# Kernel tuning notes

Hardware: AMD Instinct MI355X
Metric: run time of the kernel (lower is better)

## Reference

```python
import jax, jax.numpy as jnp
import numpy as np

MERGE_K = 3   # merge_kernel
DS_K = 3      # ds_kernel (avg-pool kernel)
STRIDE = 2


def _unfold(x, kernel, stride):
    """Torch-style F.pad + unfold(2).unfold(3): x [N,C,H,W] -> [N,Ho,Wo,K,C],
    K = kernel**2 in row-major (dh, dw) order, padding = kernel//2 with zeros."""
    pad = kernel // 2
    N, C, H, W = x.shape
    Ho, Wo = H // stride, W // stride
    xp = jnp.pad(x, ((0, 0), (0, 0), (pad, pad), (pad, pad)))
    pats = [
        xp[:, :, di:di + stride * (Ho - 1) + 1:stride,
               dj:dj + stride * (Wo - 1) + 1:stride]
        for di in range(kernel) for dj in range(kernel)
    ]
    p = jnp.stack(pats, axis=-1)          # [N,C,Ho,Wo,K]
    return p.transpose(0, 2, 3, 4, 1)     # [N,Ho,Wo,K,C]


def setup_inputs() -> dict:
    key = jax.random.key(0)
    x = jax.random.normal(key, (32, 768, 56, 56), dtype=jnp.float32)
    return {"x": x}


def reference(x):
    # compute_kq=False: k = q = x
    # AvgPool2d(3, stride=2, padding=1), count_include_pad=True -> mean over
    # zero-padded 3x3 windows == mean over K axis of the unfold.
    q = _unfold(x, DS_K, STRIDE).mean(axis=3)   # [N,Ho,Wo,C]
    kv = _unfold(x, MERGE_K, STRIDE)            # [N,Ho,Wo,K,C]; k and v are identical unfolds of x
    scores = jnp.einsum('nhwc,nhwkc->nhwk', q, kv) / MERGE_K  # divide by merge_kernel (=3), per source
    attn = jax.nn.softmax(scores, axis=-1)      # [N,Ho,Wo,K]
    y = jnp.einsum('nhwk,nhwkc->nhwc', attn, kv)  # weighted merge
    return y.transpose(0, 3, 1, 2)              # [N,C,Ho,Wo]
```

## Files before the change

### kernel.cpp

```cpp
#include <hip/hip_runtime.h>


constexpr int N_  = 32;
constexpr int C_  = 768;
constexpr int H_  = 56;
constexpr int W_  = 56;
constexpr int HO_ = 28;
constexpr int WO_ = 28;
constexpr int HW_ = H_ * W_;

constexpr int SC      = 16;
constexpr int NSUB    = C_ / SC;
constexpr int TILE_F4 = 768;

#define WAITV3() do { asm volatile("s_waitcnt vmcnt(3)" ::: "memory"); \
                      __builtin_amdgcn_sched_barrier(0); } while (0)
#define WAITV0() do { asm volatile("s_waitcnt vmcnt(0)" ::: "memory"); \
                      __builtin_amdgcn_sched_barrier(0); } while (0)
#define RAWBAR() do { asm volatile("" ::: "memory"); __builtin_amdgcn_s_barrier(); \
                      __builtin_amdgcn_sched_barrier(0); } while (0)

__global__ __launch_bounds__(256)
void fused_kernel(const float* __restrict__ x, float* __restrict__ out) {
    __shared__ float4 bufs[3][TILE_F4];
    __shared__ float  sred[8 * 252];
    __shared__ float  attn_s[252];

    const int tid  = threadIdx.x;
    const int blk  = blockIdx.x;
    const int n    = blk / HO_;
    const int ho   = blk - n * HO_;
    const int row0 = 2 * ho - 1;
    const int lane = tid & 63;
    const int wv   = tid >> 6;

    int goff[3], lds4[3];
#pragma unroll
    for (int j = 0; j < 3; ++j) {
        int q  = wv + 4 * j;
        int i  = q * 64 + lane;
        int ii = i > 671 ? 671 : i;
        int c  = ii / 42;
        int rem = ii - c * 42;
        int r  = rem / 14;
        int kk = rem - r * 14;
        int grow = row0 + r; if (grow < 0) grow = 0;
        goff[j] = c * HW_ + grow * W_ + 4 * kk;
        lds4[j] = q * 64;
    }

    const float* xb = x + (size_t)n * C_ * HW_;
    auto stage = [&](int sub, int bsel) {
        const float* xs = xb + (size_t)sub * (SC * HW_);
        float4* tb = &bufs[bsel][0];
#pragma unroll
        for (int j = 0; j < 3; ++j)
            __builtin_amdgcn_global_load_lds(
                (const __attribute__((address_space(1))) unsigned int*)(xs + goff[j]),
                (__attribute__((address_space(3))) unsigned int*)(tb + lds4[j]),
                16, 0, 0);
    };

    const int g   = tid >> 5;
    const int wo  = tid & 31;
    const bool act = wo < WO_;
    const float mt  = (ho > 0) ? 1.f : 0.f;
    const float ml  = (wo > 0) ? 1.f : 0.f;
    const float mtl = mt * ml;

    float acc[9];
#pragma unroll
    for (int k = 0; k < 9; ++k) acc[k] = 0.f;

    stage(0, 0);
    stage(1, 1);
    WAITV3();
    RAWBAR();

    for (int t = 0; t < 48; ++t) {
        int s = t + 2;
        stage(s < 48 ? s : s - 48, s % 3);
        const float* cur = (const float*)&bufs[t % 3][0];
        if (act) {
#pragma unroll
            for (int cc = 0; cc < 2; ++cc) {
                const float* tp = cur + (g * 2 + cc) * 168 + 2 * wo - 1;
                float w0 = tp[0]   * mtl, w1 = tp[1]   * mt, w2 = tp[2]   * mt;
                float w3 = tp[56]  * ml,  w4 = tp[57],      w5 = tp[58];
                float w6 = tp[112] * ml,  w7 = tp[113],     w8 = tp[114];
                float q = ((w0 + w1) + (w2 + w3)) + ((w4 + w5) + (w6 + w7)) + w8;
                acc[0] += q * w0; acc[1] += q * w1; acc[2] += q * w2;
                acc[3] += q * w3; acc[4] += q * w4; acc[5] += q * w5;
                acc[6] += q * w6; acc[7] += q * w7; acc[8] += q * w8;
            }
        }
        WAITV3();
        RAWBAR();
    }

    if (act) {
#pragma unroll
        for (int k = 0; k < 9; ++k) sred[g * 252 + wo * 9 + k] = acc[k];
    }
    __syncthreads();
    if (tid < 252) {
        float t = 0.f;
#pragma unroll
        for (int g2 = 0; g2 < 8; ++g2) t += sred[g2 * 252 + tid];
        attn_s[tid] = t * (1.f / 27.f);
    }
    __syncthreads();
    if (tid < WO_) {
        float* s = &attn_s[tid * 9];
        float v[9];
#pragma unroll
        for (int k = 0; k < 9; ++k) v[k] = s[k];
        float m = v[0];
#pragma unroll
        for (int k = 1; k < 9; ++k) m = fmaxf(m, v[k]);
        float d = 0.f;
#pragma unroll
        for (int k = 0; k < 9; ++k) { v[k] = __expf(v[k] - m); d += v[k]; }
        float inv = 1.f / d;
#pragma unroll
        for (int k = 0; k < 9; ++k) s[k] = v[k] * inv;
    }
    __syncthreads();

    const int cA = tid / 28, wA = tid - cA * 28;
    const int iB = tid + 256;
    const int cB = iB / 28, wB = iB - cB * 28;
    const bool actB = iB < 448;
    const float mlA = (wA > 0) ? 1.f : 0.f;
    const float mlB = (wB > 0) ? 1.f : 0.f;
    float* ob = out + (size_t)n * C_ * (HO_ * WO_) + (size_t)ho * WO_;

    for (int t = 48; t < 96; ++t) {
        if (t <= 93) stage(t + 2 - 48, (t + 2) % 3);
        const float* cur = (const float*)&bufs[t % 3][0];
        const int sub = t - 48;
        {
            const float* tp = cur + cA * 168 + 2 * wA - 1;
            const float* a  = &attn_s[wA * 9];
            float w0 = tp[0]   * (mt * mlA), w1 = tp[1]   * mt, w2 = tp[2] * mt;
            float w3 = tp[56]  * mlA,        w4 = tp[57],       w5 = tp[58];
            float w6 = tp[112] * mlA,        w7 = tp[113],      w8 = tp[114];
            float y = a[0]*w0 + a[1]*w1 + a[2]*w2 + a[3]*w3 + a[4]*w4
                    + a[5]*w5 + a[6]*w6 + a[7]*w7 + a[8]*w8;
            ob[(size_t)(sub * SC + cA) * (HO_ * WO_) + wA] = y;
        }
        if (actB) {
            const float* tp = cur + cB * 168 + 2 * wB - 1;
            const float* a  = &attn_s[wB * 9];
            float w0 = tp[0]   * (mt * mlB), w1 = tp[1]   * mt, w2 = tp[2] * mt;
            float w3 = tp[56]  * mlB,        w4 = tp[57],       w5 = tp[58];
            float w6 = tp[112] * mlB,        w7 = tp[113],      w8 = tp[114];
            float y = a[0]*w0 + a[1]*w1 + a[2]*w2 + a[3]*w3 + a[4]*w4
                    + a[5]*w5 + a[6]*w6 + a[7]*w7 + a[8]*w8;
            ob[(size_t)(sub * SC + cB) * (HO_ * WO_) + wB] = y;
        }
        if (t < 94) { WAITV3(); } else { WAITV0(); }
        RAWBAR();
    }
}

extern "C" void kernel_launch(void* const* d_in, const int* in_sizes, int n_in,
                              void* d_out, int out_size, void* d_ws, size_t ws_size,
                              hipStream_t stream) {
    const float* x = (const float*)d_in[0];
    float* out     = (float*)d_out;
    fused_kernel<<<dim3(N_ * HO_), dim3(256), 0, stream>>>(x, out);
}
```

Measured before the change: 566.0 us.

## Give each wave private double-buffered LDS staging and drop per-step block barriers

Each wavefront now loads and processes its own 4 channels of every 16-channel slab into a wave-private double buffer. Only a vmcnt wait is needed per step, so the block-wide s_barrier in both the score pass and the merge pass goes away. Partial scores are folded across the two half-waves with a shuffle before the cross-wave LDS reduction, which shrinks the reduction buffer. The trade-off is shallower prefetch (two buffers instead of three) and some idle lanes in the third load and in the output loop.

```diff
diff --git a/kernel.cpp b/kernel.cpp
--- a/kernel.cpp
+++ b/kernel.cpp
@@ -9,21 +9,18 @@
 constexpr int WO_ = 28;
 constexpr int HW_ = H_ * W_;
 
-constexpr int SC      = 16;
-constexpr int NSUB    = C_ / SC;
-constexpr int TILE_F4 = 768;
+constexpr int SC   = 16;
+constexpr int NSUB = C_ / SC;
 
 #define WAITV3() do { asm volatile("s_waitcnt vmcnt(3)" ::: "memory"); \
                       __builtin_amdgcn_sched_barrier(0); } while (0)
 #define WAITV0() do { asm volatile("s_waitcnt vmcnt(0)" ::: "memory"); \
                       __builtin_amdgcn_sched_barrier(0); } while (0)
-#define RAWBAR() do { asm volatile("" ::: "memory"); __builtin_amdgcn_s_barrier(); \
-                      __builtin_amdgcn_sched_barrier(0); } while (0)
 
 __global__ __launch_bounds__(256)
 void fused_kernel(const float* __restrict__ x, float* __restrict__ out) {
-    __shared__ float4 bufs[3][TILE_F4];
-    __shared__ float  sred[8 * 252];
+    __shared__ float4 bufs[4][2][168];
+    __shared__ float  sred[4 * 252];
     __shared__ float  attn_s[252];
 
     const int tid  = threadIdx.x;
@@ -34,36 +31,37 @@
     const int lane = tid & 63;
     const int wv   = tid >> 6;
 
-    int goff[3], lds4[3];
+    int goff[3];
 #pragma unroll
     for (int j = 0; j < 3; ++j) {
-        int q  = wv + 4 * j;
-        int i  = q * 64 + lane;
-        int ii = i > 671 ? 671 : i;
-        int c  = ii / 42;
-        int rem = ii - c * 42;
-        int r  = rem / 14;
-        int kk = rem - r * 14;
+        int idx = j * 64 + lane;
+        if (idx > 167) idx = 167;
+        int c   = idx / 42;
+        int rem = idx - c * 42;
+        int r   = rem / 14;
+        int kk  = rem - r * 14;
         int grow = row0 + r; if (grow < 0) grow = 0;
-        goff[j] = c * HW_ + grow * W_ + 4 * kk;
-        lds4[j] = q * 64;
+        goff[j] = (4 * wv + c) * HW_ + grow * W_ + 4 * kk;
     }
 
     const float* xb = x + (size_t)n * C_ * HW_;
-    auto stage = [&](int sub, int bsel) {
+    auto stage = [&](int sub, int b) {
         const float* xs = xb + (size_t)sub * (SC * HW_);
-        float4* tb = &bufs[bsel][0];
-#pragma unroll
-        for (int j = 0; j < 3; ++j)
+        float4* tb = &bufs[wv][b][0];
+        __builtin_amdgcn_global_load_lds(
+            (const __attribute__((address_space(1))) unsigned int*)(xs + goff[0]),
+            (__attribute__((address_space(3))) unsigned int*)(tb), 16, 0, 0);
+        __builtin_amdgcn_global_load_lds(
+            (const __attribute__((address_space(1))) unsigned int*)(xs + goff[1]),
+            (__attribute__((address_space(3))) unsigned int*)(tb + 64), 16, 0, 0);
+        if (lane < 40)
             __builtin_amdgcn_global_load_lds(
-                (const __attribute__((address_space(1))) unsigned int*)(xs + goff[j]),
-                (__attribute__((address_space(3))) unsigned int*)(tb + lds4[j]),
-                16, 0, 0);
+                (const __attribute__((address_space(1))) unsigned int*)(xs + goff[2]),
+                (__attribute__((address_space(3))) unsigned int*)(tb + 128), 16, 0, 0);
     };
 
-    const int g   = tid >> 5;
-    const int wo  = tid & 31;
-    const bool act = wo < WO_;
+    const int half = lane >> 5;
+    const int wo   = lane & 31;
     const float mt  = (ho > 0) ? 1.f : 0.f;
     const float ml  = (wo > 0) ? 1.f : 0.f;
     const float mtl = mt * ml;
@@ -73,40 +71,34 @@
     for (int k = 0; k < 9; ++k) acc[k] = 0.f;
 
     stage(0, 0);
-    stage(1, 1);
-    WAITV3();
-    RAWBAR();
-
-    for (int t = 0; t < 48; ++t) {
-        int s = t + 2;
-        stage(s < 48 ? s : s - 48, s % 3);
-        const float* cur = (const float*)&bufs[t % 3][0];
-        if (act) {
+    for (int t = 0; t < NSUB; ++t) {
+        if (t < NSUB - 1) { stage(t + 1, (t + 1) & 1); WAITV3(); }
+        else              { WAITV0(); }
+        const float* tbf = (const float*)&bufs[wv][t & 1][0];
 #pragma unroll
-            for (int cc = 0; cc < 2; ++cc) {
-                const float* tp = cur + (g * 2 + cc) * 168 + 2 * wo - 1;
-                float w0 = tp[0]   * mtl, w1 = tp[1]   * mt, w2 = tp[2]   * mt;
-                float w3 = tp[56]  * ml,  w4 = tp[57],      w5 = tp[58];
-                float w6 = tp[112] * ml,  w7 = tp[113],     w8 = tp[114];
-                float q = ((w0 + w1) + (w2 + w3)) + ((w4 + w5) + (w6 + w7)) + w8;
-                acc[0] += q * w0; acc[1] += q * w1; acc[2] += q * w2;
-                acc[3] += q * w3; acc[4] += q * w4; acc[5] += q * w5;
-                acc[6] += q * w6; acc[7] += q * w7; acc[8] += q * w8;
-            }
+        for (int cc = 0; cc < 2; ++cc) {
+            const float* tp = tbf + (half * 2 + cc) * 168 + 2 * wo - 1;
+            float w0 = tp[0]   * mtl, w1 = tp[1]   * mt, w2 = tp[2]   * mt;
+            float w3 = tp[56]  * ml,  w4 = tp[57],      w5 = tp[58];
+            float w6 = tp[112] * ml,  w7 = tp[113],     w8 = tp[114];
+            float q = ((w0 + w1) + (w2 + w3)) + ((w4 + w5) + (w6 + w7)) + w8;
+            acc[0] += q * w0; acc[1] += q * w1; acc[2] += q * w2;
+            acc[3] += q * w3; acc[4] += q * w4; acc[5] += q * w5;
+            acc[6] += q * w6; acc[7] += q * w7; acc[8] += q * w8;
         }
-        WAITV3();
-        RAWBAR();
     }
 
-    if (act) {
+    stage(0, 0);
+
 #pragma unroll
-        for (int k = 0; k < 9; ++k) sred[g * 252 + wo * 9 + k] = acc[k];
+    for (int k = 0; k < 9; ++k) acc[k] += __shfl_down(acc[k], 32);
+    if (lane < WO_) {
+#pragma unroll
+        for (int k = 0; k < 9; ++k) sred[wv * 252 + lane * 9 + k] = acc[k];
     }
     __syncthreads();
     if (tid < 252) {
-        float t = 0.f;
-#pragma unroll
-        for (int g2 = 0; g2 < 8; ++g2) t += sred[g2 * 252 + tid];
+        float t = sred[tid] + sred[252 + tid] + sred[504 + tid] + sred[756 + tid];
         attn_s[tid] = t * (1.f / 27.f);
     }
     __syncthreads();
@@ -127,40 +119,27 @@
     }
     __syncthreads();
 
-    const int cA = tid / 28, wA = tid - cA * 28;
-    const int iB = tid + 256;
-    const int cB = iB / 28, wB = iB - cB * 28;
-    const bool actB = iB < 448;
-    const float mlA = (wA > 0) ? 1.f : 0.f;
-    const float mlB = (wB > 0) ? 1.f : 0.f;
     float* ob = out + (size_t)n * C_ * (HO_ * WO_) + (size_t)ho * WO_;
-
-    for (int t = 48; t < 96; ++t) {
-        if (t <= 93) stage(t + 2 - 48, (t + 2) % 3);
-        const float* cur = (const float*)&bufs[t % 3][0];
-        const int sub = t - 48;
-        {
-            const float* tp = cur + cA * 168 + 2 * wA - 1;
-            const float* a  = &attn_s[wA * 9];
-            float w0 = tp[0]   * (mt * mlA), w1 = tp[1]   * mt, w2 = tp[2] * mt;
-            float w3 = tp[56]  * mlA,        w4 = tp[57],       w5 = tp[58];
-            float w6 = tp[112] * mlA,        w7 = tp[113],      w8 = tp[114];
-            float y = a[0]*w0 + a[1]*w1 + a[2]*w2 + a[3]*w3 + a[4]*w4
-                    + a[5]*w5 + a[6]*w6 + a[7]*w7 + a[8]*w8;
-            ob[(size_t)(sub * SC + cA) * (HO_ * WO_) + wA] = y;
+    for (int t = 0; t < NSUB; ++t) {
+        if (t < NSUB - 1) { stage(t + 1, (t + 1) & 1); WAITV3(); }
+        else              { WAITV0(); }
+        const float* tbf = (const float*)&bufs[wv][t & 1][0];
+#pragma unroll
+        for (int rep = 0; rep < 2; ++rep) {
+            int item = rep * 64 + lane;
+            if (item < 112) {
+                int c = item / 28, w = item - c * 28;
+                float mlw = (w > 0) ? 1.f : 0.f;
+                const float* tp = tbf + c * 168 + 2 * w - 1;
+                const float* a  = &attn_s[w * 9];
+                float w0 = tp[0]   * (mt * mlw), w1 = tp[1]   * mt, w2 = tp[2] * mt;
+                float w3 = tp[56]  * mlw,        w4 = tp[57],       w5 = tp[58];
+                float w6 = tp[112] * mlw,        w7 = tp[113],      w8 = tp[114];
+                float y = a[0]*w0 + a[1]*w1 + a[2]*w2 + a[3]*w3 + a[4]*w4
+                        + a[5]*w5 + a[6]*w6 + a[7]*w7 + a[8]*w8;
+                ob[(size_t)(t * SC + 4 * wv + c) * (HO_ * WO_) + w] = y;
+            }
         }
-        if (actB) {
-            const float* tp = cur + cB * 168 + 2 * wB - 1;
-            const float* a  = &attn_s[wB * 9];
-            float w0 = tp[0]   * (mt * mlB), w1 = tp[1]   * mt, w2 = tp[2] * mt;
-            float w3 = tp[56]  * mlB,        w4 = tp[57],       w5 = tp[58];
-            float w6 = tp[112] * mlB,        w7 = tp[113],      w8 = tp[114];
-            float y = a[0]*w0 + a[1]*w1 + a[2]*w2 + a[3]*w3 + a[4]*w4
-                    + a[5]*w5 + a[6]*w6 + a[7]*w7 + a[8]*w8;
-            ob[(size_t)(sub * SC + cB) * (HO_ * WO_) + wB] = y;
-        }
-        if (t < 94) { WAITV3(); } else { WAITV0(); }
-        RAWBAR();
     }
 }
 
```

Measured after the change: 521.2 us. 7.9% less time.
